# Performance work log

Measured on AMD Instinct MI355X. Metric: run time of the kernel, lower is better.

## Reference

```python
import jax, jax.numpy as jnp
import numpy as np

C = 512
GROUPS = 8
EPS = 1e-5


def setup_inputs() -> dict:
    key = jax.random.key(0)
    ks = jax.random.split(key, 7)
    b, c, h, w = 32, C, 32, 32
    x = jax.random.normal(ks[0], (b, c, h, w), dtype=jnp.float32)
    norm_gamma = jnp.ones((c,), dtype=jnp.float32)
    norm_beta = jnp.zeros((c,), dtype=jnp.float32)
    # 1x1 convs == per-pixel linear layers; store as [out, in] matrices
    qkv_w = jax.random.normal(ks[1], (3 * c, c), dtype=jnp.float32) * (1.0 / np.sqrt(c))
    qkv_b = jnp.zeros((3 * c,), dtype=jnp.float32)
    out_w = jax.random.normal(ks[2], (c, c), dtype=jnp.float32) * (1.0 / np.sqrt(c))
    out_b = jnp.zeros((c,), dtype=jnp.float32)
    return {"x": x, "norm_gamma": norm_gamma, "norm_beta": norm_beta,
            "qkv_w": qkv_w, "qkv_b": qkv_b, "out_w": out_w, "out_b": out_b}


def group_norm(x, gamma, beta):
    b, c, h, w = x.shape
    xg = x.reshape(b, GROUPS, c // GROUPS, h, w)
    mean = jnp.mean(xg, axis=(2, 3, 4), keepdims=True)
    var = jnp.var(xg, axis=(2, 3, 4), keepdims=True)
    xg = (xg - mean) * jax.lax.rsqrt(var + EPS)
    x = xg.reshape(b, c, h, w)
    return x * gamma[None, :, None, None] + beta[None, :, None, None]


def reference(x, norm_gamma, norm_beta, qkv_w, qkv_b, out_w, out_b):
    b, c, h, w = x.shape
    xn = group_norm(x, norm_gamma, norm_beta)
    # 1x1 conv: [b,c,h,w] -> [b,3c,h,w]
    qkv = jnp.einsum('oc,bchw->bohw', qkv_w, xn) + qkv_b[None, :, None, None]
    q, k, v = jnp.split(qkv.reshape(b, 3 * c, h * w), 3, axis=1)  # each [b,c,hw]
    scale = c ** (-0.5)
    attn = jnp.einsum('bci,bcj->bij', q, k) * scale  # [b, hw, hw]
    attn = jax.nn.softmax(attn, axis=-1)
    out = jnp.einsum('bij,bcj->bci', attn, v).reshape(b, c, h, w)
    out = jnp.einsum('oc,bchw->bohw', out_w, out) + out_b[None, :, None, None]
    return x + out
```

## Files before the change

kernel.cpp:

```cpp
#include <hip/hip_runtime.h>

#define HW 1024
#define CD 512

typedef __bf16 bf16x8 __attribute__((ext_vector_type(8)));
typedef float f32x4 __attribute__((ext_vector_type(4)));

__device__ __forceinline__ unsigned short f2bf(float f) {
    unsigned int u = __float_as_uint(f);
    u += 0x7fff + ((u >> 16) & 1);
    return (unsigned short)(u >> 16);
}
__device__ __forceinline__ float bf2f(unsigned short h) {
    return __uint_as_float((unsigned)h << 16);
}

#define AS1(p) ((__attribute__((address_space(1))) void*)(p))
#define AS3(p) ((__attribute__((address_space(3))) void*)(p))
#define GLD16(gp, lp) __builtin_amdgcn_global_load_lds(AS1(gp), AS3(lp), 16, 0, 0)

__global__ __launch_bounds__(256)
void gn_stats(const float* __restrict__ x, float* __restrict__ mean, float* __restrict__ rstd) {
    int bg = blockIdx.x;
    const float4* p4 = (const float4*)(x + (size_t)bg * 65536);
    int tid = threadIdx.x;
    float s = 0.f, ss = 0.f;
#pragma unroll 8
    for (int it = 0; it < 64; ++it) {
        float4 v = p4[tid + it * 256];
        s  += v.x + v.y + v.z + v.w;
        ss += v.x * v.x + v.y * v.y + v.z * v.z + v.w * v.w;
    }
#pragma unroll
    for (int d = 32; d > 0; d >>= 1) { s += __shfl_down(s, d); ss += __shfl_down(ss, d); }
    __shared__ float ls[4], lss[4];
    if ((tid & 63) == 0) { ls[tid >> 6] = s; lss[tid >> 6] = ss; }
    __syncthreads();
    if (tid == 0) {
        float S = ls[0] + ls[1] + ls[2] + ls[3];
        float SS = lss[0] + lss[1] + lss[2] + lss[3];
        float m = S * (1.f / 65536.f);
        float v = SS * (1.f / 65536.f) - m * m;
        mean[bg] = m;
        rstd[bg] = rsqrtf(v + 1e-5f);
    }
}

__global__ __launch_bounds__(256)
void gn_norm_t(const float* __restrict__ x, const float* __restrict__ mean, const float* __restrict__ rstd,
               const float* __restrict__ gamma, const float* __restrict__ beta,
               unsigned short* __restrict__ xnT) {
    __shared__ unsigned short tile[64][67];
    int i0 = blockIdx.x * 64, c0 = blockIdx.y * 64, b = blockIdx.z;
    float m = mean[b * 8 + blockIdx.y];
    float r = rstd[b * 8 + blockIdx.y];
    int tid = threadIdx.x;
    int tr = tid >> 4, tc = (tid & 15) * 4;
    const float* xb = x + ((size_t)b * CD + c0) * HW + i0;
#pragma unroll
    for (int p = 0; p < 4; ++p) {
        int c = tr + p * 16;
        float g = gamma[c0 + c] * r;
        float bb = beta[c0 + c] - m * g;
        float4 v = *(const float4*)(xb + (size_t)c * HW + tc);
        tile[c][tc + 0] = f2bf(v.x * g + bb);
        tile[c][tc + 1] = f2bf(v.y * g + bb);
        tile[c][tc + 2] = f2bf(v.z * g + bb);
        tile[c][tc + 3] = f2bf(v.w * g + bb);
    }
    __syncthreads();
    unsigned short* ob = xnT + ((size_t)b * HW + i0) * CD + c0;
#pragma unroll
    for (int p = 0; p < 4; ++p) {
        int ir = tr + p * 16;
        ushort4 u;
        u.x = tile[tc + 0][ir];
        u.y = tile[tc + 1][ir];
        u.z = tile[tc + 2][ir];
        u.w = tile[tc + 3][ir];
        *(ushort4*)(ob + (size_t)ir * CD + tc) = u;
    }
}

__global__ __launch_bounds__(256)
void tpose3_bf16(const float* __restrict__ qkv_w, unsigned short* __restrict__ dst0) {
    __shared__ unsigned short tile[64][67];
    const int zmap[3] = {0, 2, 1};
    const float* src = qkv_w + (size_t)blockIdx.z * CD * CD;
    unsigned short* dst = dst0 + (size_t)zmap[blockIdx.z] * CD * CD;
    int i0 = blockIdx.x * 64, c0 = blockIdx.y * 64;
    int tid = threadIdx.x;
    int tr = tid >> 4, tc = (tid & 15) * 4;
#pragma unroll
    for (int p = 0; p < 4; ++p) {
        int r = tr + p * 16;
        float4 v = *(const float4*)(src + (size_t)(i0 + r) * CD + c0 + tc);
        tile[r][tc + 0] = f2bf(v.x);
        tile[r][tc + 1] = f2bf(v.y);
        tile[r][tc + 2] = f2bf(v.z);
        tile[r][tc + 3] = f2bf(v.w);
    }
    __syncthreads();
#pragma unroll
    for (int p = 0; p < 4; ++p) {
        int ir = tr + p * 16;
        ushort4 u;
        u.x = tile[tc + 0][ir];
        u.y = tile[tc + 1][ir];
        u.z = tile[tc + 2][ir];
        u.w = tile[tc + 3][ir];
        *(ushort4*)(dst + (size_t)(c0 + ir) * CD + i0 + tc) = u;
    }
}

__global__ __launch_bounds__(256)
void cvt_bf16(const float* __restrict__ src, unsigned short* __restrict__ dst) {
    int i = blockIdx.x * 256 + threadIdx.x;
    float4 v = ((const float4*)src)[i];
    ushort4 u;
    u.x = f2bf(v.x); u.y = f2bf(v.y); u.z = f2bf(v.z); u.w = f2bf(v.w);
    ((ushort4*)dst)[i] = u;
}

__global__ __launch_bounds__(256)
void gvec_kernel(const float* __restrict__ wk, const float* __restrict__ bq,
                 float* __restrict__ g) {
    __shared__ float red[4][64];
    int d = blockIdx.x * 64 + (threadIdx.x & 63);
    int os = threadIdx.x >> 6;
    float acc = 0.f;
    for (int o = os * 128; o < os * 128 + 128; ++o)
        acc += wk[(size_t)o * CD + d] * bq[o];
    red[os][threadIdx.x & 63] = acc;
    __syncthreads();
    if (threadIdx.x < 64)
        g[blockIdx.x * 64 + threadIdx.x] = red[0][threadIdx.x] + red[1][threadIdx.x] +
                                           red[2][threadIdx.x] + red[3][threadIdx.x];
}

__global__ __launch_bounds__(256)
void bias2_kernel(const float* __restrict__ out_w, const float* __restrict__ bv,
                  float* __restrict__ bias2) {
    int wid = threadIdx.x >> 6, lane = threadIdx.x & 63;
    int o = blockIdx.x * 4 + wid;
    float acc = 0.f;
#pragma unroll
    for (int t = 0; t < 512; t += 64)
        acc += out_w[(size_t)o * CD + t + lane] * bv[t + lane];
#pragma unroll
    for (int d = 32; d > 0; d >>= 1) acc += __shfl_down(acc, d);
    if (lane == 0) bias2[o] = acc;
}

template<int EPI>
__global__ __launch_bounds__(256, 2)
void gemm_bt(const unsigned short* __restrict__ A, const unsigned short* __restrict__ B,
             void* __restrict__ Cv, const float* __restrict__ bias,
             int M, int N, int K, long long sA, long long sB, long long sC) {
    unsigned nx = gridDim.x, ny = gridDim.y;
    unsigned lin = blockIdx.x + nx * (blockIdx.y + ny * blockIdx.z);
    unsigned nwg = nx * ny * gridDim.z;
    unsigned work = (lin & 7) * (nwg >> 3) + (lin >> 3);
    unsigned bx = work % nx; work /= nx;
    unsigned by = work % ny;
    unsigned bz = work / ny;

    A += (size_t)bz * sA;
    B += (size_t)bz * sB;
    int m0 = by * 128, n0 = bx * 128;

    __shared__ unsigned short lA[128 * 64];
    __shared__ unsigned short lB[128 * 64];

    int tid = threadIdx.x;
    int lane = tid & 63;
    int wr = (tid >> 6) >> 1, wc = (tid >> 6) & 1;

    f32x4 acc[4][4] = {};

    int strow[4], stcol[4];
#pragma unroll
    for (int s = 0; s < 4; ++s) {
        int row = (s * 256 + tid) >> 3;
        int g = (tid & 7) ^ (row & 7);
        strow[s] = row;
        stcol[s] = g * 8;
    }

    for (int k0 = 0; k0 < K; k0 += 64) {
#pragma unroll
        for (int s = 0; s < 4; ++s) {
            GLD16(A + (size_t)(m0 + strow[s]) * K + k0 + stcol[s], lA + (size_t)(s * 256 + tid) * 8);
            GLD16(B + (size_t)(n0 + strow[s]) * K + k0 + stcol[s], lB + (size_t)(s * 256 + tid) * 8);
        }
        __syncthreads();
#pragma unroll
        for (int kk = 0; kk < 64; kk += 32) {
            bf16x8 af[4], bfr[4];
#pragma unroll
            for (int m = 0; m < 4; ++m) {
                int row = wr * 64 + m * 16 + (lane & 15);
                int off = (row * 128 + (kk + (lane >> 4) * 8) * 2) ^ ((row & 7) << 4);
                af[m] = *(const bf16x8*)((const char*)lA + off);
            }
#pragma unroll
            for (int n = 0; n < 4; ++n) {
                int row = wc * 64 + n * 16 + (lane & 15);
                int off = (row * 128 + (kk + (lane >> 4) * 8) * 2) ^ ((row & 7) << 4);
                bfr[n] = *(const bf16x8*)((const char*)lB + off);
            }
#pragma unroll
            for (int m = 0; m < 4; ++m)
#pragma unroll
                for (int n = 0; n < 4; ++n)
                    acc[m][n] = __builtin_amdgcn_mfma_f32_16x16x32_bf16(af[m], bfr[n], acc[m][n], 0, 0, 0);
        }
        __syncthreads();
    }

    int rl = (lane >> 4) * 4;
    int cl = lane & 15;
    unsigned short* Cb = (unsigned short*)Cv + (size_t)bz * sC;
#pragma unroll
    for (int m = 0; m < 4; ++m)
#pragma unroll
        for (int n = 0; n < 4; ++n) {
            int gm = m0 + wr * 64 + m * 16 + rl;
            int gn = n0 + wc * 64 + n * 16 + cl;
#pragma unroll
            for (int rg = 0; rg < 4; ++rg) {
                float v = acc[m][n][rg];
                if (EPI == 0) v += bias[gn];
                if (EPI == 1) v += bias[gm + rg];
                Cb[(size_t)(gm + rg) * N + gn] = f2bf(v);
            }
        }
}

__global__ __launch_bounds__(256, 2)
void scores_gemm(const unsigned short* __restrict__ T1, const unsigned short* __restrict__ xnT,
                 unsigned short* __restrict__ S, float* __restrict__ tmax, float* __restrict__ tsum) {
    unsigned nx = gridDim.x, ny = gridDim.y;
    unsigned lin = blockIdx.x + nx * (blockIdx.y + ny * blockIdx.z);
    unsigned nwg = nx * ny * gridDim.z;
    unsigned work = (lin & 7) * (nwg >> 3) + (lin >> 3);
    unsigned bx = work % nx; work /= nx;
    unsigned by = work % ny;
    unsigned bz = work / ny;

    const unsigned short* Ab = T1 + (size_t)bz * HW * CD;
    const unsigned short* Bb = xnT + (size_t)bz * HW * CD;
    int m0 = by * 128, n0 = bx * 128;

    __shared__ unsigned short lA[128 * 64];
    __shared__ unsigned short lB[128 * 64];
    __shared__ float redm[2][128];
    __shared__ float reds[2][128];

    int tid = threadIdx.x, lane = tid & 63;
    int wr = (tid >> 6) >> 1, wc = (tid >> 6) & 1;

    f32x4 acc[4][4] = {};
    int strow[4], stcol[4];
#pragma unroll
    for (int s = 0; s < 4; ++s) {
        int row = (s * 256 + tid) >> 3;
        int g = (tid & 7) ^ (row & 7);
        strow[s] = row;
        stcol[s] = g * 8;
    }

    for (int k0 = 0; k0 < CD; k0 += 64) {
#pragma unroll
        for (int s = 0; s < 4; ++s) {
            GLD16(Ab + (size_t)(m0 + strow[s]) * CD + k0 + stcol[s], lA + (size_t)(s * 256 + tid) * 8);
            GLD16(Bb + (size_t)(n0 + strow[s]) * CD + k0 + stcol[s], lB + (size_t)(s * 256 + tid) * 8);
        }
        __syncthreads();
#pragma unroll
        for (int kk = 0; kk < 64; kk += 32) {
            bf16x8 af[4], bfr[4];
#pragma unroll
            for (int m = 0; m < 4; ++m) {
                int row = wr * 64 + m * 16 + (lane & 15);
                int off = (row * 128 + (kk + (lane >> 4) * 8) * 2) ^ ((row & 7) << 4);
                af[m] = *(const bf16x8*)((const char*)lA + off);
            }
#pragma unroll
            for (int n = 0; n < 4; ++n) {
                int row = wc * 64 + n * 16 + (lane & 15);
                int off = (row * 128 + (kk + (lane >> 4) * 8) * 2) ^ ((row & 7) << 4);
                bfr[n] = *(const bf16x8*)((const char*)lB + off);
            }
#pragma unroll
            for (int m = 0; m < 4; ++m)
#pragma unroll
                for (int n = 0; n < 4; ++n)
                    acc[m][n] = __builtin_amdgcn_mfma_f32_16x16x32_bf16(af[m], bfr[n], acc[m][n], 0, 0, 0);
        }
        __syncthreads();
    }

    const float SL2E = 0.044194173824159216f * 1.4426950408889634f;
#pragma unroll
    for (int m = 0; m < 4; ++m)
#pragma unroll
        for (int n = 0; n < 4; ++n) acc[m][n] *= SL2E;

    int rl = (lane >> 4) * 4;
    int cl = lane & 15;

    float mr[4][4];
#pragma unroll
    for (int m = 0; m < 4; ++m)
#pragma unroll
        for (int rg = 0; rg < 4; ++rg)
            mr[m][rg] = fmaxf(fmaxf(acc[m][0][rg], acc[m][1][rg]),
                              fmaxf(acc[m][2][rg], acc[m][3][rg]));
#pragma unroll
    for (int d = 1; d < 16; d <<= 1)
#pragma unroll
        for (int m = 0; m < 4; ++m)
#pragma unroll
            for (int rg = 0; rg < 4; ++rg) mr[m][rg] = fmaxf(mr[m][rg], __shfl_xor(mr[m][rg], d));
    if ((lane & 15) == 0)
#pragma unroll
        for (int m = 0; m < 4; ++m)
#pragma unroll
            for (int rg = 0; rg < 4; ++rg) redm[wc][wr * 64 + m * 16 + rl + rg] = mr[m][rg];
    __syncthreads();
    float Mt[4][4];
#pragma unroll
    for (int m = 0; m < 4; ++m)
#pragma unroll
        for (int rg = 0; rg < 4; ++rg) {
            int row = wr * 64 + m * 16 + rl + rg;
            Mt[m][rg] = fmaxf(redm[0][row], redm[1][row]);
        }

    float sr[4][4] = {};
#pragma unroll
    for (int m = 0; m < 4; ++m)
#pragma unroll
        for (int n = 0; n < 4; ++n)
#pragma unroll
            for (int rg = 0; rg < 4; ++rg) {
                float e = __builtin_amdgcn_exp2f(acc[m][n][rg] - Mt[m][rg]);
                acc[m][n][rg] = e;
                sr[m][rg] += e;
            }
#pragma unroll
    for (int d = 1; d < 16; d <<= 1)
#pragma unroll
        for (int m = 0; m < 4; ++m)
#pragma unroll
            for (int rg = 0; rg < 4; ++rg) sr[m][rg] += __shfl_xor(sr[m][rg], d);
    if ((lane & 15) == 0)
#pragma unroll
        for (int m = 0; m < 4; ++m)
#pragma unroll
            for (int rg = 0; rg < 4; ++rg) reds[wc][wr * 64 + m * 16 + rl + rg] = sr[m][rg];
    __syncthreads();

    if (tid < 128) {
        float M = fmaxf(redm[0][tid], redm[1][tid]);
        float Z = reds[0][tid] + reds[1][tid];
        size_t o = ((size_t)bz * 8 + bx) * HW + m0 + tid;
        tmax[o] = M;
        tsum[o] = Z;
    }

    unsigned short* Sb = S + (size_t)bz * HW * HW;
#pragma unroll
    for (int m = 0; m < 4; ++m)
#pragma unroll
        for (int n = 0; n < 4; ++n) {
            int gm = m0 + wr * 64 + m * 16 + rl;
            int gn = n0 + wc * 64 + n * 16 + cl;
#pragma unroll
            for (int rg = 0; rg < 4; ++rg)
                Sb[(size_t)(gm + rg) * HW + gn] = f2bf(acc[m][n][rg]);
        }
}

__global__ __launch_bounds__(256)
void rescale_kernel(const float* __restrict__ tmax, const float* __restrict__ tsum,
                    float* __restrict__ ratio) {
    int r = blockIdx.x * 256 + threadIdx.x;
    int b = r >> 10, i = r & 1023;
    const float* tm = tmax + (size_t)b * 8 * HW + i;
    const float* ts = tsum + (size_t)b * 8 * HW + i;
    float M = -1e30f;
#pragma unroll
    for (int jt = 0; jt < 8; ++jt) M = fmaxf(M, tm[(size_t)jt * HW]);
    float Z = 0.f;
#pragma unroll
    for (int jt = 0; jt < 8; ++jt) Z += ts[(size_t)jt * HW] * __builtin_amdgcn_exp2f(tm[(size_t)jt * HW] - M);
    float rZ = 1.0f / Z;
#pragma unroll
    for (int jt = 0; jt < 7; ++jt)
        ratio[((size_t)b * 8 + jt) * HW + i] =
            __builtin_amdgcn_exp2f(tm[(size_t)jt * HW] - tm[(size_t)(jt + 1) * HW]);
    ratio[((size_t)b * 8 + 7) * HW + i] = __builtin_amdgcn_exp2f(tm[(size_t)7 * HW] - M) * rZ;
}

__global__ __launch_bounds__(256)
void pv_gemm(const unsigned short* __restrict__ A, const unsigned short* __restrict__ B,
             float* __restrict__ C, const float* __restrict__ bias,
             const float* __restrict__ resid, const float* __restrict__ ratio) {
    unsigned nx = gridDim.x, ny = gridDim.y;
    unsigned lin = blockIdx.x + nx * (blockIdx.y + ny * blockIdx.z);
    unsigned nwg = nx * ny * gridDim.z;
    unsigned work = (lin & 7) * (nwg >> 3) + (lin >> 3);
    unsigned bx = work % nx; work /= nx;
    unsigned by = work % ny;
    unsigned bz = work / ny;

    A += (size_t)bz * 512 * 1024;
    B += (size_t)bz * 1024 * 1024;
    int m0 = by * 128, n0 = bx * 128;

    __shared__ unsigned short lA[128 * 64];
    __shared__ unsigned short lB[128 * 64];

    int tid = threadIdx.x, lane = tid & 63;
    int wr = (tid >> 6) >> 1, wc = (tid >> 6) & 1;
    int cl = lane & 15;

    f32x4 acc[4][4] = {};

    int strow[4], stcol[4];
#pragma unroll
    for (int s = 0; s < 4; ++s) {
        int row = (s * 256 + tid) >> 3;
        int g = (tid & 7) ^ (row & 7);
        strow[s] = row;
        stcol[s] = g * 8;
    }

    const float* rbase = ratio + (size_t)bz * 8 * HW + n0 + wc * 64 + cl;

    for (int jt = 0; jt < 8; ++jt) {
        float r0 = rbase[(size_t)jt * HW + 0];
        float r1 = rbase[(size_t)jt * HW + 16];
        float r2 = rbase[(size_t)jt * HW + 32];
        float r3 = rbase[(size_t)jt * HW + 48];
#pragma unroll
        for (int t2 = 0; t2 < 2; ++t2) {
            int k0 = jt * 128 + t2 * 64;
#pragma unroll
            for (int s = 0; s < 4; ++s) {
                GLD16(A + (size_t)(m0 + strow[s]) * 1024 + k0 + stcol[s], lA + (size_t)(s * 256 + tid) * 8);
                GLD16(B + (size_t)(n0 + strow[s]) * 1024 + k0 + stcol[s], lB + (size_t)(s * 256 + tid) * 8);
            }
            __syncthreads();
#pragma unroll
            for (int kk = 0; kk < 64; kk += 32) {
                bf16x8 af[4], bfr[4];
#pragma unroll
                for (int m = 0; m < 4; ++m) {
                    int row = wr * 64 + m * 16 + (lane & 15);
                    int off = (row * 128 + (kk + (lane >> 4) * 8) * 2) ^ ((row & 7) << 4);
                    af[m] = *(const bf16x8*)((const char*)lA + off);
                }
#pragma unroll
                for (int n = 0; n < 4; ++n) {
                    int row = wc * 64 + n * 16 + (lane & 15);
                    int off = (row * 128 + (kk + (lane >> 4) * 8) * 2) ^ ((row & 7) << 4);
                    bfr[n] = *(const bf16x8*)((const char*)lB + off);
                }
#pragma unroll
                for (int m = 0; m < 4; ++m)
#pragma unroll
                    for (int n = 0; n < 4; ++n)
                        acc[m][n] = __builtin_amdgcn_mfma_f32_16x16x32_bf16(af[m], bfr[n], acc[m][n], 0, 0, 0);
            }
            __syncthreads();
        }
#pragma unroll
        for (int m = 0; m < 4; ++m) {
            acc[m][0] *= r0;
            acc[m][1] *= r1;
            acc[m][2] *= r2;
            acc[m][3] *= r3;
        }
    }

    int rl = (lane >> 4) * 4;
    float* Cf = C + (size_t)bz * 512 * 1024;
    const float* Rs = resid + (size_t)bz * 512 * 1024;
#pragma unroll
    for (int m = 0; m < 4; ++m)
#pragma unroll
        for (int n = 0; n < 4; ++n) {
            int gm = m0 + wr * 64 + m * 16 + rl;
            int gn = n0 + wc * 64 + n * 16 + cl;
#pragma unroll
            for (int rg = 0; rg < 4; ++rg) {
                size_t off = (size_t)(gm + rg) * 1024 + gn;
                Cf[off] = acc[m][n][rg] + bias[gm + rg] + Rs[off];
            }
        }
}

extern "C" void kernel_launch(void* const* d_in, const int* in_sizes, int n_in,
                              void* d_out, int out_size, void* d_ws, size_t ws_size,
                              hipStream_t stream) {
    const float* x      = (const float*)d_in[0];
    const float* gamma  = (const float*)d_in[1];
    const float* beta   = (const float*)d_in[2];
    const float* qkv_w  = (const float*)d_in[3];
    const float* qkv_b  = (const float*)d_in[4];
    const float* out_w  = (const float*)d_in[5];
    const float* out_b  = (const float*)d_in[6];

    char* ws = (char*)d_ws;
    unsigned short* xnT  = (unsigned short*)ws;
    unsigned short* vpr  = (unsigned short*)(ws + 33554432);
    unsigned short* SP   = (unsigned short*)(ws + 67108864);
    unsigned short* wqkT = (unsigned short*)(ws + 100663296);
    unsigned short* w2   = (unsigned short*)(ws + 101187584);
    float* gvec          = (float*)(ws + 101711872);
    float* bias2         = (float*)(ws + 101713920);
    float* meanp         = (float*)(ws + 101715968);
    float* rstdp         = (float*)(ws + 101716992);
    float* tmaxp         = (float*)(ws + 101718016);
    float* tsump         = (float*)(ws + 102766592);
    float* ratiop        = (float*)(ws + 103815168);

    unsigned short* slot0 = SP;
    unsigned short* owb   = SP + 786432;

    unsigned short* T1 = (unsigned short*)((char*)d_out + 33554432);
    float* outF = (float*)d_out;

    const float* wk_f = qkv_w + (size_t)512 * CD;

    gn_stats<<<256, 256, 0, stream>>>(x, meanp, rstdp);
    gn_norm_t<<<dim3(16, 8, 32), 256, 0, stream>>>(x, meanp, rstdp, gamma, beta, xnT);

    tpose3_bf16<<<dim3(8, 8, 3), 256, 0, stream>>>(qkv_w, slot0);
    cvt_bf16<<<256, 256, 0, stream>>>(out_w, owb);
    gvec_kernel<<<8, 256, 0, stream>>>(wk_f, qkv_b, gvec);
    bias2_kernel<<<128, 256, 0, stream>>>(out_w, qkv_b + 1024, bias2);

    gemm_bt<3><<<dim3(4, 4, 2), 256, 0, stream>>>(slot0 + 524288, slot0, wqkT, nullptr,
        512, 512, 512, 262144, 262144, 262144);

    gemm_bt<0><<<dim3(4, 8, 32), 256, 0, stream>>>(xnT, wqkT, T1, gvec,
        1024, 512, 512, 1024LL * 512, 0, 1024LL * 512);
    gemm_bt<1><<<dim3(8, 4, 32), 256, 0, stream>>>(w2, xnT, vpr, bias2,
        512, 1024, 512, 0, 1024LL * 512, 512LL * 1024);

    for (int h = 0; h < 2; ++h) {
        const unsigned short* T1h = T1 + (size_t)h * 16 * 1024 * 512;
        const unsigned short* xh  = xnT + (size_t)h * 16 * 1024 * 512;
        float* tmaxh = tmaxp + (size_t)h * 16 * 8 * 1024;
        float* tsumh = tsump + (size_t)h * 16 * 8 * 1024;

        scores_gemm<<<dim3(8, 8, 16), 256, 0, stream>>>(T1h, xh, SP, tmaxh, tsumh);
        rescale_kernel<<<64, 256, 0, stream>>>(tmaxh, tsumh, ratiop);
        pv_gemm<<<dim3(8, 4, 16), 256, 0, stream>>>(
            vpr + (size_t)h * 16 * 512 * 1024, SP,
            outF + (size_t)h * 16 * 512 * 1024, out_b,
            x + (size_t)h * 16 * 512 * 1024, ratiop);
    }
    (void)in_sizes; (void)n_in; (void)out_size; (void)ws_size;
}
```

Measured before the change: 224.8 us.

## Enlarge GEMM tiles to 256x128 with 8-wave 512-thread workgroups

The main GEMMs (QK projection, V projection, scores and PV) now use 512-thread blocks with 8 waves covering a 256x128 output tile instead of 128x128 with 4 waves. Grids are halved in the M dimension and LDS staging for A is doubled. Each loaded B tile is reused across twice as many rows, cutting global/LDS traffic per FLOP. The trade-off is more LDS per block, fewer blocks (and so possibly weaker tail balance), and a launch-bounds hint of 4 that may constrain registers. The weight-product GEMM is split into its own specialized kernel.

```diff
diff --git a/kernel.cpp b/kernel.cpp
--- a/kernel.cpp
+++ b/kernel.cpp
@@ -152,11 +152,9 @@
     if (lane == 0) bias2[o] = acc;
 }
 
-template<int EPI>
 __global__ __launch_bounds__(256, 2)
-void gemm_bt(const unsigned short* __restrict__ A, const unsigned short* __restrict__ B,
-             void* __restrict__ Cv, const float* __restrict__ bias,
-             int M, int N, int K, long long sA, long long sB, long long sC) {
+void gemm_w(const unsigned short* __restrict__ A, const unsigned short* __restrict__ B,
+            unsigned short* __restrict__ C, int K, long long sA, long long sB, long long sC) {
     unsigned nx = gridDim.x, ny = gridDim.y;
     unsigned lin = blockIdx.x + nx * (blockIdx.y + ny * blockIdx.z);
     unsigned nwg = nx * ny * gridDim.z;
@@ -172,12 +170,10 @@
     __shared__ unsigned short lA[128 * 64];
     __shared__ unsigned short lB[128 * 64];
 
-    int tid = threadIdx.x;
-    int lane = tid & 63;
+    int tid = threadIdx.x, lane = tid & 63;
     int wr = (tid >> 6) >> 1, wc = (tid >> 6) & 1;
 
     f32x4 acc[4][4] = {};
-
     int strow[4], stcol[4];
 #pragma unroll
     for (int s = 0; s < 4; ++s) {
@@ -220,7 +216,93 @@
 
     int rl = (lane >> 4) * 4;
     int cl = lane & 15;
-    unsigned short* Cb = (unsigned short*)Cv + (size_t)bz * sC;
+    unsigned short* Cb = C + (size_t)bz * sC;
+#pragma unroll
+    for (int m = 0; m < 4; ++m)
+#pragma unroll
+        for (int n = 0; n < 4; ++n) {
+            int gm = m0 + wr * 64 + m * 16 + rl;
+            int gn = n0 + wc * 64 + n * 16 + cl;
+#pragma unroll
+            for (int rg = 0; rg < 4; ++rg)
+                Cb[(size_t)(gm + rg) * 512 + gn] = f2bf(acc[m][n][rg]);
+        }
+}
+
+template<int EPI>
+__global__ __launch_bounds__(512, 4)
+void gemm_bt2(const unsigned short* __restrict__ A, const unsigned short* __restrict__ B,
+              unsigned short* __restrict__ C, const float* __restrict__ bias,
+              int M, int N, int K, long long sA, long long sB, long long sC) {
+    unsigned nx = gridDim.x, ny = gridDim.y;
+    unsigned lin = blockIdx.x + nx * (blockIdx.y + ny * blockIdx.z);
+    unsigned nwg = nx * ny * gridDim.z;
+    unsigned work = (lin & 7) * (nwg >> 3) + (lin >> 3);
+    unsigned bx = work % nx; work /= nx;
+    unsigned by = work % ny;
+    unsigned bz = work / ny;
+
+    A += (size_t)bz * sA;
+    B += (size_t)bz * sB;
+    int m0 = by * 256, n0 = bx * 128;
+
+    __shared__ unsigned short lA[256 * 64];
+    __shared__ unsigned short lB[128 * 64];
+
+    int tid = threadIdx.x, lane = tid & 63;
+    int wid = tid >> 6;
+    int wr = wid >> 1, wc = wid & 1;
+
+    f32x4 acc[4][4] = {};
+
+    int arow[4], acol[4], brow[2], bcol[2];
+#pragma unroll
+    for (int s = 0; s < 4; ++s) {
+        int idx = s * 512 + tid;
+        arow[s] = idx >> 3;
+        acol[s] = ((idx & 7) ^ (arow[s] & 7)) * 8;
+    }
+#pragma unroll
+    for (int s = 0; s < 2; ++s) {
+        int idx = s * 512 + tid;
+        brow[s] = idx >> 3;
+        bcol[s] = ((idx & 7) ^ (brow[s] & 7)) * 8;
+    }
+
+    for (int k0 = 0; k0 < K; k0 += 64) {
+#pragma unroll
+        for (int s = 0; s < 4; ++s)
+            GLD16(A + (size_t)(m0 + arow[s]) * K + k0 + acol[s], lA + (size_t)(s * 512 + tid) * 8);
+#pragma unroll
+        for (int s = 0; s < 2; ++s)
+            GLD16(B + (size_t)(n0 + brow[s]) * K + k0 + bcol[s], lB + (size_t)(s * 512 + tid) * 8);
+        __syncthreads();
+#pragma unroll
+        for (int kk = 0; kk < 64; kk += 32) {
+            int koff = (kk + (lane >> 4) * 8) * 2;
+            bf16x8 af[4], bfr[4];
+#pragma unroll
+            for (int m = 0; m < 4; ++m) {
+                int row = wr * 64 + m * 16 + (lane & 15);
+                af[m] = *(const bf16x8*)((const char*)lA + ((row * 128 + koff) ^ ((row & 7) << 4)));
+            }
+#pragma unroll
+            for (int n = 0; n < 4; ++n) {
+                int row = wc * 64 + n * 16 + (lane & 15);
+                bfr[n] = *(const bf16x8*)((const char*)lB + ((row * 128 + koff) ^ ((row & 7) << 4)));
+            }
+#pragma unroll
+            for (int m = 0; m < 4; ++m)
+#pragma unroll
+                for (int n = 0; n < 4; ++n)
+                    acc[m][n] = __builtin_amdgcn_mfma_f32_16x16x32_bf16(af[m], bfr[n], acc[m][n], 0, 0, 0);
+        }
+        __syncthreads();
+    }
+
+    int rl = (lane >> 4) * 4;
+    int cl = lane & 15;
+    unsigned short* Cb = C + (size_t)bz * sC;
 #pragma unroll
     for (int m = 0; m < 4; ++m)
 #pragma unroll
@@ -237,7 +319,7 @@
         }
 }
 
-__global__ __launch_bounds__(256, 2)
+__global__ __launch_bounds__(512, 4)
 void scores_gemm(const unsigned short* __restrict__ T1, const unsigned short* __restrict__ xnT,
                  unsigned short* __restrict__ S, float* __restrict__ tmax, float* __restrict__ tsum) {
     unsigned nx = gridDim.x, ny = gridDim.y;
@@ -250,47 +332,54 @@
 
     const unsigned short* Ab = T1 + (size_t)bz * HW * CD;
     const unsigned short* Bb = xnT + (size_t)bz * HW * CD;
-    int m0 = by * 128, n0 = bx * 128;
-
-    __shared__ unsigned short lA[128 * 64];
+    int m0 = by * 256, n0 = bx * 128;
+
+    __shared__ unsigned short lA[256 * 64];
     __shared__ unsigned short lB[128 * 64];
-    __shared__ float redm[2][128];
-    __shared__ float reds[2][128];
+    __shared__ float redm[2][256];
+    __shared__ float reds[2][256];
 
     int tid = threadIdx.x, lane = tid & 63;
-    int wr = (tid >> 6) >> 1, wc = (tid >> 6) & 1;
+    int wid = tid >> 6;
+    int wr = wid >> 1, wc = wid & 1;
 
     f32x4 acc[4][4] = {};
-    int strow[4], stcol[4];
+
+    int arow[4], acol[4], brow[2], bcol[2];
 #pragma unroll
     for (int s = 0; s < 4; ++s) {
-        int row = (s * 256 + tid) >> 3;
-        int g = (tid & 7) ^ (row & 7);
-        strow[s] = row;
-        stcol[s] = g * 8;
+        int idx = s * 512 + tid;
+        arow[s] = idx >> 3;
+        acol[s] = ((idx & 7) ^ (arow[s] & 7)) * 8;
+    }
+#pragma unroll
+    for (int s = 0; s < 2; ++s) {
+        int idx = s * 512 + tid;
+        brow[s] = idx >> 3;
+        bcol[s] = ((idx & 7) ^ (brow[s] & 7)) * 8;
     }
 
     for (int k0 = 0; k0 < CD; k0 += 64) {
 #pragma unroll
-        for (int s = 0; s < 4; ++s) {
-            GLD16(Ab + (size_t)(m0 + strow[s]) * CD + k0 + stcol[s], lA + (size_t)(s * 256 + tid) * 8);
-            GLD16(Bb + (size_t)(n0 + strow[s]) * CD + k0 + stcol[s], lB + (size_t)(s * 256 + tid) * 8);
-        }
+        for (int s = 0; s < 4; ++s)
+            GLD16(Ab + (size_t)(m0 + arow[s]) * CD + k0 + acol[s], lA + (size_t)(s * 512 + tid) * 8);
+#pragma unroll
+        for (int s = 0; s < 2; ++s)
+            GLD16(Bb + (size_t)(n0 + brow[s]) * CD + k0 + bcol[s], lB + (size_t)(s * 512 + tid) * 8);
         __syncthreads();
 #pragma unroll
         for (int kk = 0; kk < 64; kk += 32) {
+            int koff = (kk + (lane >> 4) * 8) * 2;
             bf16x8 af[4], bfr[4];
 #pragma unroll
             for (int m = 0; m < 4; ++m) {
                 int row = wr * 64 + m * 16 + (lane & 15);
-                int off = (row * 128 + (kk + (lane >> 4) * 8) * 2) ^ ((row & 7) << 4);
-                af[m] = *(const bf16x8*)((const char*)lA + off);
+                af[m] = *(const bf16x8*)((const char*)lA + ((row * 128 + koff) ^ ((row & 7) << 4)));
             }
 #pragma unroll
             for (int n = 0; n < 4; ++n) {
                 int row = wc * 64 + n * 16 + (lane & 15);
-                int off = (row * 128 + (kk + (lane >> 4) * 8) * 2) ^ ((row & 7) << 4);
-                bfr[n] = *(const bf16x8*)((const char*)lB + off);
+                bfr[n] = *(const bf16x8*)((const char*)lB + ((row * 128 + koff) ^ ((row & 7) << 4)));
             }
 #pragma unroll
             for (int m = 0; m < 4; ++m)
@@ -362,7 +451,7 @@
             for (int rg = 0; rg < 4; ++rg) reds[wc][wr * 64 + m * 16 + rl + rg] = sr[m][rg];
     __syncthreads();
 
-    if (tid < 128) {
+    if (tid < 256) {
         float M = fmaxf(redm[0][tid], redm[1][tid]);
         float Z = reds[0][tid] + reds[1][tid];
         size_t o = ((size_t)bz * 8 + bx) * HW + m0 + tid;
@@ -404,7 +493,7 @@
     ratio[((size_t)b * 8 + 7) * HW + i] = __builtin_amdgcn_exp2f(tm[(size_t)7 * HW] - M) * rZ;
 }
 
-__global__ __launch_bounds__(256)
+__global__ __launch_bounds__(512, 4)
 void pv_gemm(const unsigned short* __restrict__ A, const unsigned short* __restrict__ B,
              float* __restrict__ C, const float* __restrict__ bias,
              const float* __restrict__ resid, const float* __restrict__ ratio) {
@@ -418,24 +507,30 @@
 
     A += (size_t)bz * 512 * 1024;
     B += (size_t)bz * 1024 * 1024;
-    int m0 = by * 128, n0 = bx * 128;
-
-    __shared__ unsigned short lA[128 * 64];
+    int m0 = by * 256, n0 = bx * 128;
+
+    __shared__ unsigned short lA[256 * 64];
     __shared__ unsigned short lB[128 * 64];
 
     int tid = threadIdx.x, lane = tid & 63;
-    int wr = (tid >> 6) >> 1, wc = (tid >> 6) & 1;
+    int wid = tid >> 6;
+    int wr = wid >> 1, wc = wid & 1;
     int cl = lane & 15;
 
     f32x4 acc[4][4] = {};
 
-    int strow[4], stcol[4];
+    int arow[4], acol[4], brow[2], bcol[2];
 #pragma unroll
     for (int s = 0; s < 4; ++s) {
-        int row = (s * 256 + tid) >> 3;
-        int g = (tid & 7) ^ (row & 7);
-        strow[s] = row;
-        stcol[s] = g * 8;
+        int idx = s * 512 + tid;
+        arow[s] = idx >> 3;
+        acol[s] = ((idx & 7) ^ (arow[s] & 7)) * 8;
+    }
+#pragma unroll
+    for (int s = 0; s < 2; ++s) {
+        int idx = s * 512 + tid;
+        brow[s] = idx >> 3;
+        bcol[s] = ((idx & 7) ^ (brow[s] & 7)) * 8;
     }
 
     const float* rbase = ratio + (size_t)bz * 8 * HW + n0 + wc * 64 + cl;
@@ -449,25 +544,25 @@
         for (int t2 = 0; t2 < 2; ++t2) {
             int k0 = jt * 128 + t2 * 64;
 #pragma unroll
-            for (int s = 0; s < 4; ++s) {
-                GLD16(A + (size_t)(m0 + strow[s]) * 1024 + k0 + stcol[s], lA + (size_t)(s * 256 + tid) * 8);
-                GLD16(B + (size_t)(n0 + strow[s]) * 1024 + k0 + stcol[s], lB + (size_t)(s * 256 + tid) * 8);
-            }
+            for (int s = 0; s < 4; ++s)
+                GLD16(A + (size_t)(m0 + arow[s]) * 1024 + k0 + acol[s], lA + (size_t)(s * 512 + tid) * 8);
+#pragma unroll
+            for (int s = 0; s < 2; ++s)
+                GLD16(B + (size_t)(n0 + brow[s]) * 1024 + k0 + bcol[s], lB + (size_t)(s * 512 + tid) * 8);
             __syncthreads();
 #pragma unroll
             for (int kk = 0; kk < 64; kk += 32) {
+                int koff = (kk + (lane >> 4) * 8) * 2;
                 bf16x8 af[4], bfr[4];
 #pragma unroll
                 for (int m = 0; m < 4; ++m) {
                     int row = wr * 64 + m * 16 + (lane & 15);
-                    int off = (row * 128 + (kk + (lane >> 4) * 8) * 2) ^ ((row & 7) << 4);
-                    af[m] = *(const bf16x8*)((const char*)lA + off);
+                    af[m] = *(const bf16x8*)((const char*)lA + ((row * 128 + koff) ^ ((row & 7) << 4)));
                 }
 #pragma unroll
                 for (int n = 0; n < 4; ++n) {
                     int row = wc * 64 + n * 16 + (lane & 15);
-                    int off = (row * 128 + (kk + (lane >> 4) * 8) * 2) ^ ((row & 7) << 4);
-                    bfr[n] = *(const bf16x8*)((const char*)lB + off);
+                    bfr[n] = *(const bf16x8*)((const char*)lB + ((row * 128 + koff) ^ ((row & 7) << 4)));
                 }
 #pragma unroll
                 for (int m = 0; m < 4; ++m)
@@ -544,12 +639,12 @@
     gvec_kernel<<<8, 256, 0, stream>>>(wk_f, qkv_b, gvec);
     bias2_kernel<<<128, 256, 0, stream>>>(out_w, qkv_b + 1024, bias2);
 
-    gemm_bt<3><<<dim3(4, 4, 2), 256, 0, stream>>>(slot0 + 524288, slot0, wqkT, nullptr,
-        512, 512, 512, 262144, 262144, 262144);
-
-    gemm_bt<0><<<dim3(4, 8, 32), 256, 0, stream>>>(xnT, wqkT, T1, gvec,
+    gemm_w<<<dim3(4, 4, 2), 256, 0, stream>>>(slot0 + 524288, slot0, wqkT,
+        512, 262144, 262144, 262144);
+
+    gemm_bt2<0><<<dim3(4, 4, 32), 512, 0, stream>>>(xnT, wqkT, T1, gvec,
         1024, 512, 512, 1024LL * 512, 0, 1024LL * 512);
-    gemm_bt<1><<<dim3(8, 4, 32), 256, 0, stream>>>(w2, xnT, vpr, bias2,
+    gemm_bt2<1><<<dim3(8, 2, 32), 512, 0, stream>>>(w2, xnT, vpr, bias2,
         512, 1024, 512, 0, 1024LL * 512, 512LL * 1024);
 
     for (int h = 0; h < 2; ++h) {
@@ -558,9 +653,9 @@
         float* tmaxh = tmaxp + (size_t)h * 16 * 8 * 1024;
         float* tsumh = tsump + (size_t)h * 16 * 8 * 1024;
 
-        scores_gemm<<<dim3(8, 8, 16), 256, 0, stream>>>(T1h, xh, SP, tmaxh, tsumh);
+        scores_gemm<<<dim3(8, 4, 16), 512, 0, stream>>>(T1h, xh, SP, tmaxh, tsumh);
         rescale_kernel<<<64, 256, 0, stream>>>(tmaxh, tsumh, ratiop);
-        pv_gemm<<<dim3(8, 4, 16), 256, 0, stream>>>(
+        pv_gemm<<<dim3(8, 2, 16), 512, 0, stream>>>(
             vpr + (size_t)h * 16 * 512 * 1024, SP,
             outF + (size_t)h * 16 * 512 * 1024, out_b,
             x + (size_t)h * 16 * 512 * 1024, ratiop);
```

Result: slower. 276.6 us (+23.0%).

## Double-buffer LDS tiles in all three GEMM kernels to overlap loads with MFMA

Applied to the files above, without the earlier changes.

Adds a second LDS buffer for the A and B tiles in gemm_bt, scores_gemm and pv_gemm. The async global-to-LDS load of the next K-tile is issued before the MFMA work on the current tile, so memory latency can hide behind compute. The per-iteration syncs drop from two to one. This doubles LDS use to 64KB per block, which may limit residency to 2 blocks per CU. It also relies on the async loads completing before the single barrier at the end of each iteration.

```diff
diff --git a/kernel.cpp b/kernel.cpp
--- a/kernel.cpp
+++ b/kernel.cpp
@@ -169,8 +169,8 @@
     B += (size_t)bz * sB;
     int m0 = by * 128, n0 = bx * 128;
 
-    __shared__ unsigned short lA[128 * 64];
-    __shared__ unsigned short lB[128 * 64];
+    __shared__ unsigned short lA[2][128 * 64];
+    __shared__ unsigned short lB[2][128 * 64];
 
     int tid = threadIdx.x;
     int lane = tid & 63;
@@ -187,13 +187,22 @@
         stcol[s] = g * 8;
     }
 
-    for (int k0 = 0; k0 < K; k0 += 64) {
+    auto stage = [&](int buf, int k0) {
 #pragma unroll
         for (int s = 0; s < 4; ++s) {
-            GLD16(A + (size_t)(m0 + strow[s]) * K + k0 + stcol[s], lA + (size_t)(s * 256 + tid) * 8);
-            GLD16(B + (size_t)(n0 + strow[s]) * K + k0 + stcol[s], lB + (size_t)(s * 256 + tid) * 8);
-        }
-        __syncthreads();
+            GLD16(A + (size_t)(m0 + strow[s]) * K + k0 + stcol[s], &lA[buf][(size_t)(s * 256 + tid) * 8]);
+            GLD16(B + (size_t)(n0 + strow[s]) * K + k0 + stcol[s], &lB[buf][(size_t)(s * 256 + tid) * 8]);
+        }
+    };
+
+    int NT = K >> 6;
+    stage(0, 0);
+    __syncthreads();
+    int cur = 0;
+    for (int t = 0; t < NT; ++t) {
+        if (t + 1 < NT) stage(cur ^ 1, (t + 1) << 6);
+        const char* pa = (const char*)lA[cur];
+        const char* pb = (const char*)lB[cur];
 #pragma unroll
         for (int kk = 0; kk < 64; kk += 32) {
             bf16x8 af[4], bfr[4];
@@ -201,13 +210,13 @@
             for (int m = 0; m < 4; ++m) {
                 int row = wr * 64 + m * 16 + (lane & 15);
                 int off = (row * 128 + (kk + (lane >> 4) * 8) * 2) ^ ((row & 7) << 4);
-                af[m] = *(const bf16x8*)((const char*)lA + off);
+                af[m] = *(const bf16x8*)(pa + off);
             }
 #pragma unroll
             for (int n = 0; n < 4; ++n) {
                 int row = wc * 64 + n * 16 + (lane & 15);
                 int off = (row * 128 + (kk + (lane >> 4) * 8) * 2) ^ ((row & 7) << 4);
-                bfr[n] = *(const bf16x8*)((const char*)lB + off);
+                bfr[n] = *(const bf16x8*)(pb + off);
             }
 #pragma unroll
             for (int m = 0; m < 4; ++m)
@@ -216,6 +225,7 @@
                     acc[m][n] = __builtin_amdgcn_mfma_f32_16x16x32_bf16(af[m], bfr[n], acc[m][n], 0, 0, 0);
         }
         __syncthreads();
+        cur ^= 1;
     }
 
     int rl = (lane >> 4) * 4;
@@ -252,8 +262,8 @@
     const unsigned short* Bb = xnT + (size_t)bz * HW * CD;
     int m0 = by * 128, n0 = bx * 128;
 
-    __shared__ unsigned short lA[128 * 64];
-    __shared__ unsigned short lB[128 * 64];
+    __shared__ unsigned short lA[2][128 * 64];
+    __shared__ unsigned short lB[2][128 * 64];
     __shared__ float redm[2][128];
     __shared__ float reds[2][128];
 
@@ -270,13 +280,21 @@
         stcol[s] = g * 8;
     }
 
-    for (int k0 = 0; k0 < CD; k0 += 64) {
+    auto stage = [&](int buf, int k0) {
 #pragma unroll
         for (int s = 0; s < 4; ++s) {
-            GLD16(Ab + (size_t)(m0 + strow[s]) * CD + k0 + stcol[s], lA + (size_t)(s * 256 + tid) * 8);
-            GLD16(Bb + (size_t)(n0 + strow[s]) * CD + k0 + stcol[s], lB + (size_t)(s * 256 + tid) * 8);
-        }
-        __syncthreads();
+            GLD16(Ab + (size_t)(m0 + strow[s]) * CD + k0 + stcol[s], &lA[buf][(size_t)(s * 256 + tid) * 8]);
+            GLD16(Bb + (size_t)(n0 + strow[s]) * CD + k0 + stcol[s], &lB[buf][(size_t)(s * 256 + tid) * 8]);
+        }
+    };
+
+    stage(0, 0);
+    __syncthreads();
+    int cur = 0;
+    for (int t = 0; t < 8; ++t) {
+        if (t < 7) stage(cur ^ 1, (t + 1) << 6);
+        const char* pa = (const char*)lA[cur];
+        const char* pb = (const char*)lB[cur];
 #pragma unroll
         for (int kk = 0; kk < 64; kk += 32) {
             bf16x8 af[4], bfr[4];
@@ -284,13 +302,13 @@
             for (int m = 0; m < 4; ++m) {
                 int row = wr * 64 + m * 16 + (lane & 15);
                 int off = (row * 128 + (kk + (lane >> 4) * 8) * 2) ^ ((row & 7) << 4);
-                af[m] = *(const bf16x8*)((const char*)lA + off);
+                af[m] = *(const bf16x8*)(pa + off);
             }
 #pragma unroll
             for (int n = 0; n < 4; ++n) {
                 int row = wc * 64 + n * 16 + (lane & 15);
                 int off = (row * 128 + (kk + (lane >> 4) * 8) * 2) ^ ((row & 7) << 4);
-                bfr[n] = *(const bf16x8*)((const char*)lB + off);
+                bfr[n] = *(const bf16x8*)(pb + off);
             }
 #pragma unroll
             for (int m = 0; m < 4; ++m)
@@ -299,6 +317,7 @@
                     acc[m][n] = __builtin_amdgcn_mfma_f32_16x16x32_bf16(af[m], bfr[n], acc[m][n], 0, 0, 0);
         }
         __syncthreads();
+        cur ^= 1;
     }
 
     const float SL2E = 0.044194173824159216f * 1.4426950408889634f;
@@ -420,8 +439,8 @@
     B += (size_t)bz * 1024 * 1024;
     int m0 = by * 128, n0 = bx * 128;
 
-    __shared__ unsigned short lA[128 * 64];
-    __shared__ unsigned short lB[128 * 64];
+    __shared__ unsigned short lA[2][128 * 64];
+    __shared__ unsigned short lB[2][128 * 64];
 
     int tid = threadIdx.x, lane = tid & 63;
     int wr = (tid >> 6) >> 1, wc = (tid >> 6) & 1;
@@ -438,51 +457,62 @@
         stcol[s] = g * 8;
     }
 
+    auto stage = [&](int buf, int k0) {
+#pragma unroll
+        for (int s = 0; s < 4; ++s) {
+            GLD16(A + (size_t)(m0 + strow[s]) * 1024 + k0 + stcol[s], &lA[buf][(size_t)(s * 256 + tid) * 8]);
+            GLD16(B + (size_t)(n0 + strow[s]) * 1024 + k0 + stcol[s], &lB[buf][(size_t)(s * 256 + tid) * 8]);
+        }
+    };
+
     const float* rbase = ratio + (size_t)bz * 8 * HW + n0 + wc * 64 + cl;
 
-    for (int jt = 0; jt < 8; ++jt) {
-        float r0 = rbase[(size_t)jt * HW + 0];
-        float r1 = rbase[(size_t)jt * HW + 16];
-        float r2 = rbase[(size_t)jt * HW + 32];
-        float r3 = rbase[(size_t)jt * HW + 48];
-#pragma unroll
-        for (int t2 = 0; t2 < 2; ++t2) {
-            int k0 = jt * 128 + t2 * 64;
-#pragma unroll
-            for (int s = 0; s < 4; ++s) {
-                GLD16(A + (size_t)(m0 + strow[s]) * 1024 + k0 + stcol[s], lA + (size_t)(s * 256 + tid) * 8);
-                GLD16(B + (size_t)(n0 + strow[s]) * 1024 + k0 + stcol[s], lB + (size_t)(s * 256 + tid) * 8);
-            }
-            __syncthreads();
-#pragma unroll
-            for (int kk = 0; kk < 64; kk += 32) {
-                bf16x8 af[4], bfr[4];
-#pragma unroll
-                for (int m = 0; m < 4; ++m) {
-                    int row = wr * 64 + m * 16 + (lane & 15);
-                    int off = (row * 128 + (kk + (lane >> 4) * 8) * 2) ^ ((row & 7) << 4);
-                    af[m] = *(const bf16x8*)((const char*)lA + off);
-                }
-#pragma unroll
-                for (int n = 0; n < 4; ++n) {
-                    int row = wc * 64 + n * 16 + (lane & 15);
-                    int off = (row * 128 + (kk + (lane >> 4) * 8) * 2) ^ ((row & 7) << 4);
-                    bfr[n] = *(const bf16x8*)((const char*)lB + off);
-                }
-#pragma unroll
-                for (int m = 0; m < 4; ++m)
-#pragma unroll
-                    for (int n = 0; n < 4; ++n)
-                        acc[m][n] = __builtin_amdgcn_mfma_f32_16x16x32_bf16(af[m], bfr[n], acc[m][n], 0, 0, 0);
-            }
-            __syncthreads();
-        }
-#pragma unroll
-        for (int m = 0; m < 4; ++m) {
-            acc[m][0] *= r0;
-            acc[m][1] *= r1;
-            acc[m][2] *= r2;
-            acc[m][3] *= r3;
+    stage(0, 0);
+    __syncthreads();
+    int cur = 0;
+    float r0 = 0.f, r1 = 0.f, r2 = 0.f, r3 = 0.f;
+    for (int t = 0; t < 16; ++t) {
+        if (t + 1 < 16) stage(cur ^ 1, (t + 1) << 6);
+        if (!(t & 1)) {
+            int jt = t >> 1;
+            r0 = rbase[(size_t)jt * HW + 0];
+            r1 = rbase[(size_t)jt * HW + 16];
+            r2 = rbase[(size_t)jt * HW + 32];
+            r3 = rbase[(size_t)jt * HW + 48];
+        }
+        const char* pa = (const char*)lA[cur];
+        const char* pb = (const char*)lB[cur];
+#pragma unroll
+        for (int kk = 0; kk < 64; kk += 32) {
+            bf16x8 af[4], bfr[4];
+#pragma unroll
+            for (int m = 0; m < 4; ++m) {
+                int row = wr * 64 + m * 16 + (lane & 15);
+                int off = (row * 128 + (kk + (lane >> 4) * 8) * 2) ^ ((row & 7) << 4);
+                af[m] = *(const bf16x8*)(pa + off);
+            }
+#pragma unroll
+            for (int n = 0; n < 4; ++n) {
+                int row = wc * 64 + n * 16 + (lane & 15);
+                int off = (row * 128 + (kk + (lane >> 4) * 8) * 2) ^ ((row & 7) << 4);
+                bfr[n] = *(const bf16x8*)(pb + off);
+            }
+#pragma unroll
+            for (int m = 0; m < 4; ++m)
+#pragma unroll
+                for (int n = 0; n < 4; ++n)
+                    acc[m][n] = __builtin_amdgcn_mfma_f32_16x16x32_bf16(af[m], bfr[n], acc[m][n], 0, 0, 0);
+        }
+        __syncthreads();
+        cur ^= 1;
+        if (t & 1) {
+#pragma unroll
+            for (int m = 0; m < 4; ++m) {
+                acc[m][0] *= r0;
+                acc[m][1] *= r1;
+                acc[m][2] *= r2;
+                acc[m][3] *= r3;
+            }
         }
     }
 
```

Measured after the change: 222.9 us. About the same (-0.9%).
